# Optimization experiments

Hardware: AMD Instinct MI355X
Metric: run time of the kernel (lower is better)

Reference implementation:

```python
import jax, jax.numpy as jnp
import numpy as np

N, E, D_IN, D_EDGE = 50000, 800000, 128, 3


def setup_inputs() -> dict:
    key = jax.random.key(0)
    ks = jax.random.split(key, 24)
    p = lambda k, shape, s=0.1: (jax.random.normal(k, shape) * s).astype(jnp.float32)
    return {
        "x": jax.random.normal(ks[0], (N, D_IN), jnp.float32),
        "edge_index": jax.random.randint(ks[1], (2, E), 0, N, dtype=jnp.int32),
        "edge_attr": jax.random.normal(ks[2], (E, D_EDGE), jnp.float32),
        # layer 1: in=128, heads=4, out=64
        "W1": p(ks[3], (D_IN, 256)), "a_src1": p(ks[4], (4, 64)), "a_dst1": p(ks[5], (4, 64)),
        "We1": p(ks[6], (D_EDGE, 256)), "a_e1": p(ks[7], (4, 64)), "b1": jnp.zeros(256, jnp.float32),
        # layer 2: in=256, heads=2, out=32
        "W2": p(ks[8], (256, 64)), "a_src2": p(ks[9], (2, 32)), "a_dst2": p(ks[10], (2, 32)),
        "We2": p(ks[11], (D_EDGE, 64)), "a_e2": p(ks[12], (2, 32)), "b2": jnp.zeros(64, jnp.float32),
        # layer 3: in=64, heads=1, out=16
        "W3": p(ks[13], (64, 16)), "a_src3": p(ks[14], (1, 16)), "a_dst3": p(ks[15], (1, 16)),
        "We3": p(ks[16], (D_EDGE, 16)), "a_e3": p(ks[17], (1, 16)), "b3": jnp.zeros(16, jnp.float32),
    }


def _add_self_loops(src, dst, eattr, n):
    # PyG add_self_loops(fill_value='mean'): loop edge_attr = mean of incoming edge_attr per node
    deg = jax.ops.segment_sum(jnp.ones(src.shape[0], eattr.dtype), dst, num_segments=n)
    mean_attr = jax.ops.segment_sum(eattr, dst, num_segments=n) / jnp.maximum(deg, 1.0)[:, None]
    loop = jnp.arange(n, dtype=src.dtype)
    return (jnp.concatenate([src, loop]), jnp.concatenate([dst, loop]),
            jnp.concatenate([eattr, mean_attr], axis=0))


def _gat_layer(x, src, dst, eattr, W, a_src, a_dst, We, a_e, b):
    H, Oc = a_src.shape
    n = x.shape[0]
    xp = (x @ W).reshape(n, H, Oc)              # [N,H,O] projected nodes
    ep = (eattr @ We).reshape(-1, H, Oc)        # [E,H,O] projected edge attrs
    alpha = ((xp * a_src).sum(-1)[src]          # [E,H] attention logits
             + (xp * a_dst).sum(-1)[dst]
             + (ep * a_e).sum(-1))
    alpha = jnp.where(alpha > 0, alpha, 0.2 * alpha)  # LeakyReLU(0.2)
    m = jax.ops.segment_max(alpha, dst, num_segments=n)  # per-dst softmax (stable)
    ea = jnp.exp(alpha - m[dst])
    att = ea / jax.ops.segment_sum(ea, dst, num_segments=n)[dst]
    agg = jax.ops.segment_sum(xp[src] * att[:, :, None], dst, num_segments=n)
    return agg.reshape(n, H * Oc) + b


def reference(x, edge_index, edge_attr,
              W1, a_src1, a_dst1, We1, a_e1, b1,
              W2, a_src2, a_dst2, We2, a_e2, b2,
              W3, a_src3, a_dst3, We3, a_e3, b3):
    n = x.shape[0]
    src, dst, ea = _add_self_loops(edge_index[0], edge_index[1], edge_attr, n)
    h = jax.nn.elu(_gat_layer(x, src, dst, ea, W1, a_src1, a_dst1, We1, a_e1, b1))
    h = jax.nn.elu(_gat_layer(h, src, dst, ea, W2, a_src2, a_dst2, We2, a_e2, b2))
    return _gat_layer(h, src, dst, ea, W3, a_src3, a_dst3, We3, a_e3, b3)
```

## Files before the change

### kernel.cpp

```cpp
#include <hip/hip_runtime.h>


constexpr int NN  = 50000;
constexpr int NE  = 800000;
constexpr int NET = NE + NN;

typedef __attribute__((ext_vector_type(8))) short bf16x8;
typedef __attribute__((ext_vector_type(4))) float f32x4;

static __device__ __forceinline__ unsigned short f2bf(float f) {
  unsigned u = __float_as_uint(f);
  unsigned r = (u + 0x7FFFu + ((u >> 16) & 1u)) >> 16;
  return (unsigned short)r;
}
static __device__ __forceinline__ float bf2f(unsigned short b) {
  return __uint_as_float((unsigned)b << 16);
}


__global__ __launch_bounds__(256) void k_count(const int* __restrict__ ei,
                                               int* __restrict__ cnt) {
  int e = blockIdx.x * 256 + threadIdx.x;
  if (e >= NE) return;
  atomicAdd(&cnt[ei[NE + e]], 1);
}

__global__ __launch_bounds__(256) void k_scan1(const int* __restrict__ cnt,
                                               int* __restrict__ bsum) {
  __shared__ int lds[256];
  int base = blockIdx.x * 1024;
  int s = 0;
  for (int i = 0; i < 4; i++) {
    int idx = base + threadIdx.x * 4 + i;
    if (idx < NN) s += cnt[idx] + 1;
  }
  lds[threadIdx.x] = s;
  __syncthreads();
  for (int off = 128; off > 0; off >>= 1) {
    if (threadIdx.x < off) lds[threadIdx.x] += lds[threadIdx.x + off];
    __syncthreads();
  }
  if (threadIdx.x == 0) bsum[blockIdx.x] = lds[0];
}

__global__ void k_scan2(int* bsum, int nblk) {
  int run = 0;
  for (int i = 0; i < nblk; i++) { int v = bsum[i]; bsum[i] = run; run += v; }
}

__global__ __launch_bounds__(256) void k_scan3(const int* __restrict__ cnt,
                                               const int* __restrict__ bsum,
                                               int* __restrict__ rowp,
                                               int* __restrict__ cursor) {
  __shared__ int lds[256];
  int t = threadIdx.x;
  int base = blockIdx.x * 1024;
  int v[4];
  int s = 0;
  for (int i = 0; i < 4; i++) {
    int idx = base + t * 4 + i;
    v[i] = (idx < NN) ? cnt[idx] + 1 : 0;
    s += v[i];
  }
  lds[t] = s;
  __syncthreads();
  for (int off = 1; off < 256; off <<= 1) {
    int add = (t >= off) ? lds[t - off] : 0;
    __syncthreads();
    lds[t] += add;
    __syncthreads();
  }
  int p = bsum[blockIdx.x] + lds[t] - s;
  for (int i = 0; i < 4; i++) {
    int idx = base + t * 4 + i;
    if (idx < NN) { rowp[idx] = p; cursor[idx] = p; }
    p += v[i];
  }
  if (blockIdx.x == 0 && t == 0) rowp[NN] = NET;
}

__global__ __launch_bounds__(256) void k_scatter(const int* __restrict__ ei,
                                                 const float* __restrict__ ea,
                                                 int* __restrict__ cursor,
                                                 int4* __restrict__ sorted) {
  int e = blockIdx.x * 256 + threadIdx.x;
  if (e >= NE) return;
  int s = ei[e];
  int d = ei[NE + e];
  int pos = atomicAdd(&cursor[d], 1);
  int4 r;
  r.x = s;
  r.y = __float_as_int(ea[3 * (size_t)e + 0]);
  r.z = __float_as_int(ea[3 * (size_t)e + 1]);
  r.w = __float_as_int(ea[3 * (size_t)e + 2]);
  sorted[pos] = r;
}

__global__ __launch_bounds__(256) void k_segloop(const int* __restrict__ rowp,
                                                 int4* __restrict__ sorted) {
  int t = threadIdx.x, g = t >> 4, gl = t & 15;
  int n = blockIdx.x * 16 + g;
  if (n >= NN) return;
  int rp0 = rowp[n], rp1e = rowp[n + 1] - 1;
  float s0 = 0.f, s1 = 0.f, s2 = 0.f;
  for (int j = rp0 + gl; j < rp1e; j += 16) {
    int4 r = sorted[j];
    s0 += __int_as_float(r.y);
    s1 += __int_as_float(r.z);
    s2 += __int_as_float(r.w);
  }
#pragma unroll
  for (int off = 8; off > 0; off >>= 1) {
    s0 += __shfl_xor(s0, off);
    s1 += __shfl_xor(s1, off);
    s2 += __shfl_xor(s2, off);
  }
  if (gl == 0) {
    float inv = 1.f / fmaxf((float)(rp1e - rp0), 1.f);
    int4 r;
    r.x = n;
    r.y = __float_as_int(s0 * inv);
    r.z = __float_as_int(s1 * inv);
    r.w = __float_as_int(s2 * inv);
    sorted[rp1e] = r;
  }
}

__global__ __launch_bounds__(256) void k_cast(const float* __restrict__ in,
                                              unsigned short* __restrict__ out,
                                              int n4) {
  int i = blockIdx.x * 256 + threadIdx.x;
  if (i >= n4) return;
  float4 v = ((const float4*)in)[i];
  ushort4 b;
  b.x = f2bf(v.x); b.y = f2bf(v.y); b.z = f2bf(v.z); b.w = f2bf(v.w);
  ((ushort4*)out)[i] = b;
}

template <int K, int BN>
__global__ __launch_bounds__(256) void k_gemm_mfma(const unsigned short* __restrict__ A,
                                                   const float* __restrict__ W,
                                                   float* __restrict__ C,
                                                   unsigned short* __restrict__ Cb,
                                                   int M, int NC) {
  constexpr int NT = BN / 16;
  constexpr int LGBN = (BN == 64) ? 6 : 4;
  __shared__ unsigned short Wt[BN][K + 8];
  const int t = threadIdx.x;
  const int row0 = blockIdx.x * 64;
  const int col0 = blockIdx.y * BN;
  for (int idx = t; idx < BN * K; idx += 256) {
    int c = idx & (BN - 1);
    int k = idx >> LGBN;
    Wt[c][k] = f2bf(W[(size_t)k * NC + col0 + c]);
  }
  __syncthreads();
  const int wave = t >> 6, lane = t & 63;
  const int rbase = row0 + wave * 16 + (lane & 15);
  const int kgrp = (lane >> 4) * 8;
  const bool rok = rbase < M;
  f32x4 acc[NT];
#pragma unroll
  for (int i = 0; i < NT; i++) acc[i] = f32x4{0.f, 0.f, 0.f, 0.f};
#pragma unroll
  for (int kk = 0; kk < K; kk += 32) {
    bf16x8 a = {};
    if (rok) a = *(const bf16x8*)(A + (size_t)rbase * K + kk + kgrp);
#pragma unroll
    for (int nt = 0; nt < NT; nt++) {
      bf16x8 b = *(const bf16x8*)(&Wt[nt * 16 + (lane & 15)][kk + kgrp]);
      acc[nt] = __builtin_amdgcn_mfma_f32_16x16x32_bf16(a, b, acc[nt], 0, 0, 0);
    }
  }
  const int wr0 = row0 + wave * 16 + (lane >> 4) * 4;
  const int wc = lane & 15;
#pragma unroll
  for (int nt = 0; nt < NT; nt++) {
#pragma unroll
    for (int i = 0; i < 4; i++) {
      int r = wr0 + i;
      if (r < M) {
        float v = acc[nt][i];
        C[(size_t)r * NC + col0 + nt * 16 + wc] = v;
        Cb[(size_t)r * NC + col0 + nt * 16 + wc] = f2bf(v);
      }
    }
  }
}

template <int H, int O>
__global__ __launch_bounds__(256) void k_scores(const float* __restrict__ xp,
                                                const float* __restrict__ a_src,
                                                const float* __restrict__ a_dst,
                                                float* __restrict__ ssrc,
                                                float* __restrict__ sdst) {
  constexpr int HO = H * O;
  constexpr int NPB = 256 / HO;
  int t = threadIdx.x;
  int j = t % HO;
  int n = blockIdx.x * NPB + t / HO;
  if (n >= NN) return;
  float v = xp[(size_t)n * HO + j];
  float ps = v * a_src[j];
  float pd = v * a_dst[j];
#pragma unroll
  for (int off = O / 2; off > 0; off >>= 1) {
    ps += __shfl_xor(ps, off);
    pd += __shfl_xor(pd, off);
  }
  if ((j & (O - 1)) == 0) {
    int h = j / O;
    ssrc[n * H + h] = ps;
    sdst[n * H + h] = pd;
  }
}

template <int H, int O>
__global__ void k_ce(const float* __restrict__ We, const float* __restrict__ ae,
                     float* __restrict__ c) {
  int t = threadIdx.x;
  if (t >= 3 * H) return;
  int d = t / H, h = t % H;
  float s = 0.f;
  for (int o = 0; o < O; o++) s += We[d * (H * O) + h * O + o] * ae[h * O + o];
  c[t] = s;
}

template <int H, int V, bool DO_ELU, bool OB16>
__global__ __launch_bounds__(256) void k_agg2(const int4* __restrict__ sorted,
                                              const int* __restrict__ rowp,
                                              const unsigned short* __restrict__ xpb,
                                              const float* __restrict__ ssrc,
                                              const float* __restrict__ sdst,
                                              const float* __restrict__ ce,
                                              const float* __restrict__ bias,
                                              void* __restrict__ out) {
  constexpr int HO = 64 * V;
  constexpr int OC = HO / H;
  __shared__ float lds_p[4][64][H];
  __shared__ int lds_s[4][64];
  const int wave = threadIdx.x >> 6, lane = threadIdx.x & 63;
  const int n = blockIdx.x * 4 + wave;
  if (n >= NN) return;
  const int rp0 = rowp[n], rp1 = rowp[n + 1];
  const int h_lane = (lane * V) / OC;

  float sd[H], c0[H], c1[H], c2[H];
#pragma unroll
  for (int h = 0; h < H; h++) {
    sd[h] = sdst[n * H + h];
    c0[h] = ce[h];
    c1[h] = ce[H + h];
    c2[h] = ce[2 * H + h];
  }

  float den[H];
#pragma unroll
  for (int h = 0; h < H; h++) den[h] = 0.f;
  float acc[V];
#pragma unroll
  for (int i = 0; i < V; i++) acc[i] = 0.f;

  for (int cbase = rp0; cbase < rp1; cbase += 64) {
    const int cnt = min(64, rp1 - cbase);
    if (lane < cnt) {
      int4 r = sorted[cbase + lane];
      int s = r.x;
      float e0 = __int_as_float(r.y), e1 = __int_as_float(r.z), e2 = __int_as_float(r.w);
      float sv[H];
      if constexpr (H == 4) {
        float4 v = *(const float4*)(ssrc + 4 * (size_t)s);
        sv[0] = v.x; sv[1] = v.y; sv[2] = v.z; sv[3] = v.w;
      } else if constexpr (H == 2) {
        float2 v = *(const float2*)(ssrc + 2 * (size_t)s);
        sv[0] = v.x; sv[1] = v.y;
      } else {
        sv[0] = ssrc[s];
      }
#pragma unroll
      for (int h = 0; h < H; h++) {
        float a = sv[h] + sd[h] + e0 * c0[h] + e1 * c1[h] + e2 * c2[h];
        a = a > 0.f ? a : 0.2f * a;
        float p = __expf(a);
        den[h] += p;
        lds_p[wave][lane][h] = p;
      }
      lds_s[wave][lane] = s;
    }
    for (int c = 0; c < cnt; c++) {
      const float pw = lds_p[wave][c][h_lane];
      const int s = lds_s[wave][c];
      const unsigned short* row = xpb + (size_t)s * HO + lane * V;
      if constexpr (V == 4) {
        ushort4 u = *(const ushort4*)row;
        acc[0] += pw * bf2f(u.x);
        acc[1] += pw * bf2f(u.y);
        acc[2] += pw * bf2f(u.z);
        acc[3] += pw * bf2f(u.w);
      } else {
        acc[0] += pw * bf2f(row[0]);
      }
    }
  }
#pragma unroll
  for (int off = 32; off > 0; off >>= 1)
#pragma unroll
    for (int h = 0; h < H; h++) den[h] += __shfl_xor(den[h], off);

  const float dinv = 1.f / den[h_lane];
#pragma unroll
  for (int i = 0; i < V; i++) {
    const int jc = lane * V + i;
    float v = acc[i] * dinv + bias[jc];
    if constexpr (DO_ELU) v = v > 0.f ? v : __expf(v) - 1.f;
    if constexpr (OB16) {
      ((unsigned short*)out)[(size_t)n * HO + jc] = f2bf(v);
    } else {
      ((float*)out)[(size_t)n * HO + jc] = v;
    }
  }
}

__global__ __launch_bounds__(256) void k_agg3(const int4* __restrict__ sorted,
                                              const int* __restrict__ rowp,
                                              const unsigned short* __restrict__ xpb,
                                              const float* __restrict__ ssrc,
                                              const float* __restrict__ sdst,
                                              const float* __restrict__ ce,
                                              const float* __restrict__ bias,
                                              float* __restrict__ out) {
  __shared__ float lds_p[16][16];
  __shared__ int lds_s[16][16];
  int t = threadIdx.x, g = t >> 4, gl = t & 15;
  int n = blockIdx.x * 16 + g;
  if (n >= NN) return;
  int rp0 = rowp[n], rp1 = rowp[n + 1];
  float sd = sdst[n], ce0 = ce[0], ce1 = ce[1], ce2 = ce[2];

  float den = 0.f, acc = 0.f;
  for (int cbase = rp0; cbase < rp1; cbase += 16) {
    int cnt = min(16, rp1 - cbase);
    if (gl < cnt) {
      int4 r = sorted[cbase + gl];
      float a = ssrc[r.x] + sd + __int_as_float(r.y) * ce0 +
                __int_as_float(r.z) * ce1 + __int_as_float(r.w) * ce2;
      a = a > 0.f ? a : 0.2f * a;
      float p = __expf(a);
      den += p;
      lds_p[g][gl] = p;
      lds_s[g][gl] = r.x;
    }
    for (int c = 0; c < cnt; c++)
      acc += lds_p[g][c] * bf2f(xpb[(size_t)lds_s[g][c] * 16 + gl]);
  }
#pragma unroll
  for (int off = 8; off > 0; off >>= 1) den += __shfl_xor(den, off);
  out[(size_t)n * 16 + gl] = acc / den + bias[gl];
}


extern "C" void kernel_launch(void* const* d_in, const int* in_sizes, int n_in,
                              void* d_out, int out_size, void* d_ws, size_t ws_size,
                              hipStream_t stream) {
  const float* x   = (const float*)d_in[0];
  const int*   ei  = (const int*)d_in[1];
  const float* ea  = (const float*)d_in[2];
  const float* W1  = (const float*)d_in[3];
  const float* as1 = (const float*)d_in[4];
  const float* ad1 = (const float*)d_in[5];
  const float* We1 = (const float*)d_in[6];
  const float* ae1 = (const float*)d_in[7];
  const float* b1  = (const float*)d_in[8];
  const float* W2  = (const float*)d_in[9];
  const float* as2 = (const float*)d_in[10];
  const float* ad2 = (const float*)d_in[11];
  const float* We2 = (const float*)d_in[12];
  const float* ae2 = (const float*)d_in[13];
  const float* b2  = (const float*)d_in[14];
  const float* W3  = (const float*)d_in[15];
  const float* as3 = (const float*)d_in[16];
  const float* ad3 = (const float*)d_in[17];
  const float* We3 = (const float*)d_in[18];
  const float* ae3 = (const float*)d_in[19];
  const float* b3  = (const float*)d_in[20];
  float* out = (float*)d_out;

  char* base = (char*)d_ws;
  size_t off = 0;
  auto get = [&](size_t bytes) -> char* {
    char* q = base + off;
    off += (bytes + 255) & ~(size_t)255;
    return q;
  };
  int*   cnt    = (int*)get((size_t)NN * 4);
  int*   rowp   = (int*)get((size_t)(NN + 1) * 4);
  int*   cursor = (int*)get((size_t)NN * 4);
  int*   bsum   = (int*)get(256 * 4);
  int4*  sorted = (int4*)get((size_t)NET * 16);
  float* ssrc   = (float*)get((size_t)NN * 16);
  float* sdst   = (float*)get((size_t)NN * 16);
  float* ce     = (float*)get(256);
  float* bufA   = (float*)get((size_t)NN * 256 * 4);
  unsigned short* xb  = (unsigned short*)get((size_t)NN * 256 * 2);
  unsigned short* x16 = (unsigned short*)get((size_t)NN * 128 * 2);
  unsigned short* h1b = (unsigned short*)get((size_t)NN * 256 * 2);
  unsigned short* h2b = (unsigned short*)get((size_t)NN * 64 * 2);
  (void)ws_size; (void)in_sizes; (void)n_in; (void)out_size;

  hipMemsetAsync(cnt, 0, (size_t)NN * 4, stream);

  const int EB = (NE + 255) / 256;
  const int SB = (NN + 1023) / 1024;

  k_count<<<EB, 256, 0, stream>>>(ei, cnt);
  k_scan1<<<SB, 256, 0, stream>>>(cnt, bsum);
  k_scan2<<<1, 1, 0, stream>>>(bsum, SB);
  k_scan3<<<SB, 256, 0, stream>>>(cnt, bsum, rowp, cursor);
  k_scatter<<<EB, 256, 0, stream>>>(ei, ea, cursor, sorted);
  k_segloop<<<(NN + 15) / 16, 256, 0, stream>>>(rowp, sorted);

  const int GR64 = (NN + 63) / 64;
  const int AGB = (NN + 3) / 4;

  k_cast<<<(NN * 128 / 4 + 255) / 256, 256, 0, stream>>>(x, x16, NN * 128 / 4);

  k_gemm_mfma<128, 64><<<dim3(GR64, 4), 256, 0, stream>>>(x16, W1, bufA, xb, NN, 256);
  k_scores<4, 64><<<NN, 256, 0, stream>>>(bufA, as1, ad1, ssrc, sdst);
  k_ce<4, 64><<<1, 64, 0, stream>>>(We1, ae1, ce);
  k_agg2<4, 4, true, true><<<AGB, 256, 0, stream>>>(sorted, rowp, xb, ssrc, sdst, ce, b1, (void*)h1b);

  k_gemm_mfma<256, 64><<<dim3(GR64, 1), 256, 0, stream>>>(h1b, W2, bufA, xb, NN, 64);
  k_scores<2, 32><<<(NN + 3) / 4, 256, 0, stream>>>(bufA, as2, ad2, ssrc, sdst);
  k_ce<2, 32><<<1, 64, 0, stream>>>(We2, ae2, ce);
  k_agg2<2, 1, true, true><<<AGB, 256, 0, stream>>>(sorted, rowp, xb, ssrc, sdst, ce, b2, (void*)h2b);

  k_gemm_mfma<64, 16><<<dim3(GR64, 1), 256, 0, stream>>>(h2b, W3, bufA, xb, NN, 16);
  k_scores<1, 16><<<(NN + 15) / 16, 256, 0, stream>>>(bufA, as3, ad3, ssrc, sdst);
  k_ce<1, 16><<<1, 64, 0, stream>>>(We3, ae3, ce);
  k_agg3<<<(NN + 15) / 16, 256, 0, stream>>>(sorted, rowp, xb, ssrc, sdst, ce, b3, out);
}
```

Baseline: 427.2 us.

## Fuse attention-score computation and input cast into MFMA GEMM epilogue

The per-layer score kernels are folded into the GEMM epilogue. It now reduces the accumulator against a_src/a_dst with lane shuffles and writes ssrc/sdst directly, so the fp32 projected buffer no longer needs to be written and read back. Layer 1 converts the fp32 input to bf16 inside the GEMM, which removes the separate cast kernel. The three edge-constant kernels are merged into one launch. The costs are more register pressure in the GEMM and scores computed from unrounded fp32 accumulators, as before.

```diff
diff --git a/kernel.cpp b/kernel.cpp
--- a/kernel.cpp
+++ b/kernel.cpp
@@ -126,37 +126,54 @@
   }
 }
 
-__global__ __launch_bounds__(256) void k_cast(const float* __restrict__ in,
-                                              unsigned short* __restrict__ out,
-                                              int n4) {
-  int i = blockIdx.x * 256 + threadIdx.x;
-  if (i >= n4) return;
-  float4 v = ((const float4*)in)[i];
-  ushort4 b;
-  b.x = f2bf(v.x); b.y = f2bf(v.y); b.z = f2bf(v.z); b.w = f2bf(v.w);
-  ((ushort4*)out)[i] = b;
-}
-
-template <int K, int BN>
-__global__ __launch_bounds__(256) void k_gemm_mfma(const unsigned short* __restrict__ A,
-                                                   const float* __restrict__ W,
-                                                   float* __restrict__ C,
-                                                   unsigned short* __restrict__ Cb,
-                                                   int M, int NC) {
+__global__ void k_ce_all(const float* __restrict__ We1, const float* __restrict__ ae1,
+                         const float* __restrict__ We2, const float* __restrict__ ae2,
+                         const float* __restrict__ We3, const float* __restrict__ ae3,
+                         float* __restrict__ ce) {
+  int t = threadIdx.x;
+  if (t < 12) {
+    int d = t / 4, h = t % 4;
+    float s = 0.f;
+    for (int o = 0; o < 64; o++) s += We1[d * 256 + h * 64 + o] * ae1[h * 64 + o];
+    ce[t] = s;
+  } else if (t >= 16 && t < 22) {
+    int u = t - 16, d = u / 2, h = u % 2;
+    float s = 0.f;
+    for (int o = 0; o < 32; o++) s += We2[d * 64 + h * 32 + o] * ae2[h * 32 + o];
+    ce[t] = s;
+  } else if (t >= 24 && t < 27) {
+    int d = t - 24;
+    float s = 0.f;
+    for (int o = 0; o < 16; o++) s += We3[d * 16 + o] * ae3[o];
+    ce[t] = s;
+  }
+}
+
+template <int K, int BN, int O, bool AFP32>
+__global__ __launch_bounds__(256) void k_gemm_sc(const void* __restrict__ Ap,
+                                                 const float* __restrict__ W,
+                                                 unsigned short* __restrict__ Cb,
+                                                 const float* __restrict__ a_src,
+                                                 const float* __restrict__ a_dst,
+                                                 float* __restrict__ ssrc,
+                                                 float* __restrict__ sdst,
+                                                 int M, int NC) {
   constexpr int NT = BN / 16;
-  constexpr int LGBN = (BN == 64) ? 6 : 4;
+  constexpr int HL = BN / O;
   __shared__ unsigned short Wt[BN][K + 8];
   const int t = threadIdx.x;
   const int row0 = blockIdx.x * 64;
   const int col0 = blockIdx.y * BN;
+  const int H = NC / O;
   for (int idx = t; idx < BN * K; idx += 256) {
-    int c = idx & (BN - 1);
-    int k = idx >> LGBN;
+    int c = idx % BN;
+    int k = idx / BN;
     Wt[c][k] = f2bf(W[(size_t)k * NC + col0 + c]);
   }
   __syncthreads();
   const int wave = t >> 6, lane = t & 63;
-  const int rbase = row0 + wave * 16 + (lane & 15);
+  const int wc = lane & 15;
+  const int rbase = row0 + wave * 16 + wc;
   const int kgrp = (lane >> 4) * 8;
   const bool rok = rbase < M;
   f32x4 acc[NT];
@@ -165,65 +182,70 @@
 #pragma unroll
   for (int kk = 0; kk < K; kk += 32) {
     bf16x8 a = {};
-    if (rok) a = *(const bf16x8*)(A + (size_t)rbase * K + kk + kgrp);
+    if (rok) {
+      if constexpr (AFP32) {
+        const float* Af = (const float*)Ap;
+        float4 v0 = *(const float4*)(Af + (size_t)rbase * K + kk + kgrp);
+        float4 v1 = *(const float4*)(Af + (size_t)rbase * K + kk + kgrp + 4);
+        a[0] = (short)f2bf(v0.x); a[1] = (short)f2bf(v0.y);
+        a[2] = (short)f2bf(v0.z); a[3] = (short)f2bf(v0.w);
+        a[4] = (short)f2bf(v1.x); a[5] = (short)f2bf(v1.y);
+        a[6] = (short)f2bf(v1.z); a[7] = (short)f2bf(v1.w);
+      } else {
+        a = *(const bf16x8*)((const unsigned short*)Ap + (size_t)rbase * K + kk + kgrp);
+      }
+    }
 #pragma unroll
     for (int nt = 0; nt < NT; nt++) {
-      bf16x8 b = *(const bf16x8*)(&Wt[nt * 16 + (lane & 15)][kk + kgrp]);
+      bf16x8 b = *(const bf16x8*)(&Wt[nt * 16 + wc][kk + kgrp]);
       acc[nt] = __builtin_amdgcn_mfma_f32_16x16x32_bf16(a, b, acc[nt], 0, 0, 0);
     }
   }
   const int wr0 = row0 + wave * 16 + (lane >> 4) * 4;
-  const int wc = lane & 15;
+  float psrc[4][HL], pdst[4][HL];
+#pragma unroll
+  for (int i = 0; i < 4; i++)
+#pragma unroll
+    for (int hl = 0; hl < HL; hl++) { psrc[i][hl] = 0.f; pdst[i][hl] = 0.f; }
 #pragma unroll
   for (int nt = 0; nt < NT; nt++) {
+    const int col = col0 + nt * 16 + wc;
+    const float asv = a_src[col];
+    const float adv = a_dst[col];
+    constexpr int dummy = 0; (void)dummy;
+    const int hl = (nt * 16) / O;
+#pragma unroll
+    for (int i = 0; i < 4; i++) {
+      int r = wr0 + i;
+      float v = acc[nt][i];
+      if (r < M) Cb[(size_t)r * NC + col] = f2bf(v);
+      psrc[i][hl] += v * asv;
+      pdst[i][hl] += v * adv;
+    }
+  }
+#pragma unroll
+  for (int off = 1; off < 16; off <<= 1)
+#pragma unroll
+    for (int i = 0; i < 4; i++)
+#pragma unroll
+      for (int hl = 0; hl < HL; hl++) {
+        psrc[i][hl] += __shfl_xor(psrc[i][hl], off);
+        pdst[i][hl] += __shfl_xor(pdst[i][hl], off);
+      }
+  if (wc == 0) {
 #pragma unroll
     for (int i = 0; i < 4; i++) {
       int r = wr0 + i;
       if (r < M) {
-        float v = acc[nt][i];
-        C[(size_t)r * NC + col0 + nt * 16 + wc] = v;
-        Cb[(size_t)r * NC + col0 + nt * 16 + wc] = f2bf(v);
-      }
-    }
-  }
-}
-
-template <int H, int O>
-__global__ __launch_bounds__(256) void k_scores(const float* __restrict__ xp,
-                                                const float* __restrict__ a_src,
-                                                const float* __restrict__ a_dst,
-                                                float* __restrict__ ssrc,
-                                                float* __restrict__ sdst) {
-  constexpr int HO = H * O;
-  constexpr int NPB = 256 / HO;
-  int t = threadIdx.x;
-  int j = t % HO;
-  int n = blockIdx.x * NPB + t / HO;
-  if (n >= NN) return;
-  float v = xp[(size_t)n * HO + j];
-  float ps = v * a_src[j];
-  float pd = v * a_dst[j];
-#pragma unroll
-  for (int off = O / 2; off > 0; off >>= 1) {
-    ps += __shfl_xor(ps, off);
-    pd += __shfl_xor(pd, off);
-  }
-  if ((j & (O - 1)) == 0) {
-    int h = j / O;
-    ssrc[n * H + h] = ps;
-    sdst[n * H + h] = pd;
-  }
-}
-
-template <int H, int O>
-__global__ void k_ce(const float* __restrict__ We, const float* __restrict__ ae,
-                     float* __restrict__ c) {
-  int t = threadIdx.x;
-  if (t >= 3 * H) return;
-  int d = t / H, h = t % H;
-  float s = 0.f;
-  for (int o = 0; o < O; o++) s += We[d * (H * O) + h * O + o] * ae[h * O + o];
-  c[t] = s;
+#pragma unroll
+        for (int hl = 0; hl < HL; hl++) {
+          int h = col0 / O + hl;
+          ssrc[r * H + h] = psrc[i][hl];
+          sdst[r * H + h] = pdst[i][hl];
+        }
+      }
+    }
+  }
 }
 
 template <int H, int V, bool DO_ELU, bool OB16>
@@ -400,9 +422,7 @@
   float* ssrc   = (float*)get((size_t)NN * 16);
   float* sdst   = (float*)get((size_t)NN * 16);
   float* ce     = (float*)get(256);
-  float* bufA   = (float*)get((size_t)NN * 256 * 4);
   unsigned short* xb  = (unsigned short*)get((size_t)NN * 256 * 2);
-  unsigned short* x16 = (unsigned short*)get((size_t)NN * 128 * 2);
   unsigned short* h1b = (unsigned short*)get((size_t)NN * 256 * 2);
   unsigned short* h2b = (unsigned short*)get((size_t)NN * 64 * 2);
   (void)ws_size; (void)in_sizes; (void)n_in; (void)out_size;
@@ -418,24 +438,20 @@
   k_scan3<<<SB, 256, 0, stream>>>(cnt, bsum, rowp, cursor);
   k_scatter<<<EB, 256, 0, stream>>>(ei, ea, cursor, sorted);
   k_segloop<<<(NN + 15) / 16, 256, 0, stream>>>(rowp, sorted);
+  k_ce_all<<<1, 64, 0, stream>>>(We1, ae1, We2, ae2, We3, ae3, ce);
 
   const int GR64 = (NN + 63) / 64;
   const int AGB = (NN + 3) / 4;
 
-  k_cast<<<(NN * 128 / 4 + 255) / 256, 256, 0, stream>>>(x, x16, NN * 128 / 4);
-
-  k_gemm_mfma<128, 64><<<dim3(GR64, 4), 256, 0, stream>>>(x16, W1, bufA, xb, NN, 256);
-  k_scores<4, 64><<<NN, 256, 0, stream>>>(bufA, as1, ad1, ssrc, sdst);
-  k_ce<4, 64><<<1, 64, 0, stream>>>(We1, ae1, ce);
+  k_gemm_sc<128, 64, 64, true><<<dim3(GR64, 4), 256, 0, stream>>>(
+      (const void*)x, W1, xb, as1, ad1, ssrc, sdst, NN, 256);
   k_agg2<4, 4, true, true><<<AGB, 256, 0, stream>>>(sorted, rowp, xb, ssrc, sdst, ce, b1, (void*)h1b);
 
-  k_gemm_mfma<256, 64><<<dim3(GR64, 1), 256, 0, stream>>>(h1b, W2, bufA, xb, NN, 64);
-  k_scores<2, 32><<<(NN + 3) / 4, 256, 0, stream>>>(bufA, as2, ad2, ssrc, sdst);
-  k_ce<2, 32><<<1, 64, 0, stream>>>(We2, ae2, ce);
-  k_agg2<2, 1, true, true><<<AGB, 256, 0, stream>>>(sorted, rowp, xb, ssrc, sdst, ce, b2, (void*)h2b);
-
-  k_gemm_mfma<64, 16><<<dim3(GR64, 1), 256, 0, stream>>>(h2b, W3, bufA, xb, NN, 16);
-  k_scores<1, 16><<<(NN + 15) / 16, 256, 0, stream>>>(bufA, as3, ad3, ssrc, sdst);
-  k_ce<1, 16><<<1, 64, 0, stream>>>(We3, ae3, ce);
-  k_agg3<<<(NN + 15) / 16, 256, 0, stream>>>(sorted, rowp, xb, ssrc, sdst, ce, b3, out);
-}
+  k_gemm_sc<256, 64, 32, false><<<dim3(GR64, 1), 256, 0, stream>>>(
+      (const void*)h1b, W2, xb, as2, ad2, ssrc, sdst, NN, 64);
+  k_agg2<2, 1, true, true><<<AGB, 256, 0, stream>>>(sorted, rowp, xb, ssrc, sdst, ce + 16, b2, (void*)h2b);
+
+  k_gemm_sc<64, 16, 16, false><<<dim3(GR64, 1), 256, 0, stream>>>(
+      (const void*)h2b, W3, xb, as3, ad3, ssrc, sdst, NN, 16);
+  k_agg3<<<(NN + 15) / 16, 256, 0, stream>>>(sorted, rowp, xb, ssrc, sdst, ce + 24, b3, out);
+}
```

Result: faster. 392.2 us (-8.2%).
